# Performance work log

Measured on AMD Instinct MI355X. Metric: run time of the kernel, lower is better.

## Reference

```python
import jax, jax.numpy as jnp
import numpy as np

T, B, D, H, A = 256, 512, 128, 128, 8
RUN_COUNT = 1000

def _orth(k, shape, scale):
    w = jax.random.normal(k, shape, jnp.float32)
    q, r = jnp.linalg.qr(w)
    q = q * jnp.sign(jnp.diag(r))[None, :]
    return scale * q

def setup_inputs() -> dict:
    key = jax.random.key(0)
    ks = jax.random.split(key, 12)
    return {
        'hidden': jnp.zeros((B, H), jnp.float32),
        'obs': jax.random.normal(ks[0], (T, B, D), jnp.float32),
        'dones': (jax.random.randint(ks[1], (T, B), 0, 10) == 0),
        'mean_obs': jax.random.normal(ks[2], (D,), jnp.float32) * 0.1,
        'welford_S': jax.random.uniform(ks[3], (D,), jnp.float32) * RUN_COUNT,
        'running_count': RUN_COUNT,
        'W_emb': _orth(ks[4], (D, H), float(np.sqrt(2.0))), 'b_emb': jnp.zeros((H,), jnp.float32),
        'Wi': jax.random.normal(ks[5], (H, 3 * H), jnp.float32) / np.sqrt(H),
        'Wh': jax.random.normal(ks[6], (H, 3 * H), jnp.float32) / np.sqrt(H),
        'bh': jnp.zeros((3 * H,), jnp.float32),
        'W_act': _orth(ks[7], (H, H), 2.0), 'b_act': jnp.zeros((H,), jnp.float32),
        'W_alpha': _orth(ks[8], (H, A), 0.01), 'b_alpha': jnp.zeros((A,), jnp.float32),
        'W_beta': _orth(ks[9], (H, A), 0.01), 'b_beta': jnp.zeros((A,), jnp.float32),
    }

def _welford(M0, S0, count0, xs):
    # sequential Welford update over stacked rows, as in the original lax.scan
    def step(carry, x):
        M, S, c = carry
        c = c + 1.0
        M_new = M + (x - M) / c
        S_new = S + (x - M) * (x - M_new)
        return (M_new, S_new, c), None
    (M, S, c), _ = jax.lax.scan(step, (M0, S0, jnp.asarray(count0, jnp.float32)), xs)
    return M, S, c

def reference(hidden, obs, dones, mean_obs, welford_S, running_count,
              W_emb, b_emb, Wi, Wh, bh, W_act, b_act, W_alpha, b_alpha, W_beta, b_beta):
    # --- running-stat normalization (running_count > 0 branch) ---
    stacked = obs.reshape(-1, obs.shape[-1])  # [T*B, D]
    M, S, c = _welford(mean_obs, welford_S, running_count, stacked)
    var = S / (c - 1.0)
    obs_n = (obs - M) / (jnp.sqrt(var) + 1e-8)
    # --- embedding MLP ---
    emb = jax.nn.relu(obs_n @ W_emb + b_emb)  # [T, B, H]
    # --- GRU scan over time; precompute input-side gate projections (no input bias, flax GRUCell) ---
    xg = emb @ Wi  # [T, B, 3H]
    def gru_step(h, inp):
        x3, reset = inp
        h = jnp.where(reset[:, None], 0.0, h)  # reset carry where done
        hg = h @ Wh + bh
        xr, xz, xn = jnp.split(x3, 3, axis=-1)
        hr, hz, hn = jnp.split(hg, 3, axis=-1)
        r = jax.nn.sigmoid(xr + hr)
        z = jax.nn.sigmoid(xz + hz)
        n = jnp.tanh(xn + r * hn)
        h_new = (1.0 - z) * n + z * h
        return h_new, h_new
    h_last, ys = jax.lax.scan(gru_step, hidden, (xg, dones))  # ys: [T, B, H]
    # --- policy heads ---
    act = jax.nn.relu(ys @ W_act + b_act)
    alpha = jax.nn.softplus(act @ W_alpha + b_alpha) + 1.0
    beta = jax.nn.softplus(act @ W_beta + b_beta) + 1.0
    return h_last, alpha, beta, M, S
```

## Files before the change

### kernel.cpp

```cpp
#include <hip/hip_runtime.h>

#define T_DIM 256
#define B_DIM 512
#define D_DIM 128
#define H_DIM 128
#define A_DIM 8
#define N_ROWS (T_DIM*B_DIM)
#define NT (N_ROWS/16)
#define NWIN 8
#define WLEN 32
#define LOG2E 1.4426950408889634f

typedef __attribute__((ext_vector_type(4))) float f32x4;
typedef __attribute__((ext_vector_type(8))) short bf16x8;
typedef __attribute__((ext_vector_type(4))) short bf16x4;
typedef __attribute__((ext_vector_type(8))) _Float16 f16x8;
typedef __attribute__((ext_vector_type(4))) unsigned u32x4;
typedef __attribute__((ext_vector_type(2))) unsigned u32x2;

#define OFF_PSUM   0ull
#define OFF_PSQ    1048576ull
#define OFF_STATM  2097152ull
#define OFF_STATI  2097664ull
#define OFF_WEMB   2098176ull
#define OFF_WI     2130944ull
#define OFF_WH     2229248ull
#define OFF_WACT   2425856ull
#define OFF_WHEAD  2458624ull
#define OFF_TLO    2462720ull
#define OFF_UH     2464768ull
#define OFF_XG     4194304ull
#define OFF_YS     104857600ull

#define OUT_H      0
#define OUT_ALPHA  65536
#define OUT_BETA   1114112
#define OUT_M      2162688
#define OUT_S      2162816

__device__ inline short f2bf(float x){
  union { float f; unsigned u; } v; v.f = x;
  unsigned r = v.u + 0x7FFFu + ((v.u>>16)&1u);
  return (short)(r>>16);
}
__device__ inline float bf2f(short h){
  union { unsigned u; float f; } v; v.u = ((unsigned)(unsigned short)h)<<16; return v.f;
}

__device__ inline int swz(int row, int col){ return row*136 + col; }

__device__ inline unsigned cvtpk_bf16(float lo, float hi){
  unsigned r;
  asm("v_cvt_pk_bf16_f32 %0, %1, %2" : "=v"(r) : "v"(lo), "v"(hi));
  return r;
}

__global__ __launch_bounds__(256) void k_partial(const float* __restrict__ obs,
                                                 double* __restrict__ psum,
                                                 double* __restrict__ psq){
  int tid = threadIdx.x; int col = tid & 127; int rh = tid >> 7;
  double s = 0.0, q = 0.0;
  for (int r = blockIdx.x*2 + rh; r < N_ROWS; r += 2048){
    float v = obs[(size_t)r*D_DIM + col];
    s += (double)v; q += (double)v*(double)v;
  }
  __shared__ double ls[256], lq[256];
  ls[tid]=s; lq[tid]=q; __syncthreads();
  if (rh==0){
    psum[(size_t)blockIdx.x*128 + col] = ls[tid] + ls[tid+128];
    psq [(size_t)blockIdx.x*128 + col] = lq[tid] + lq[tid+128];
  }
}

__global__ __launch_bounds__(1024) void k_stats(const double* __restrict__ psum,
                                                const double* __restrict__ psq,
                                                const float* __restrict__ mean_obs,
                                                const float* __restrict__ welfS,
                                                const int* __restrict__ runcnt,
                                                float* __restrict__ outM, float* __restrict__ outS,
                                                float* __restrict__ wsM,  float* __restrict__ wsI){
  int tid = threadIdx.x; int col = tid & 127; int seg = tid >> 7;
  double s=0.0, q=0.0;
  for (int b=seg; b<1024; b+=8){ s += psum[(size_t)b*128+col]; q += psq[(size_t)b*128+col]; }
  __shared__ double ls[1024], lq[1024];
  ls[tid]=s; lq[tid]=q; __syncthreads();
  if (seg==0){
    for (int b=1;b<8;b++){ s += ls[b*128+col]; q += lq[b*128+col]; }
    double c0 = (double)runcnt[0];
    double Nn = (double)N_ROWS;
    double n  = c0 + Nn;
    double M0 = (double)mean_obs[col], S0 = (double)welfS[col];
    double mb = s / Nn;
    double delta = mb - M0;
    double M = M0 + delta * Nn / n;
    double M2b = q - Nn*mb*mb;
    double S = S0 + M2b + delta*delta*c0*Nn/n;
    double var = S / (n - 1.0);
    float inv = (float)(1.0/(sqrt(var)+1e-8));
    outM[col] = (float)M; outS[col] = (float)S;
    wsM[col]  = (float)M; wsI[col]  = inv;
  }
}

__global__ void k_pack_all(const float* __restrict__ W_emb, const float* __restrict__ Wi,
                           const float* __restrict__ Wh,    const float* __restrict__ W_act,
                           const float* __restrict__ W_al,  const float* __restrict__ W_be,
                           short* __restrict__ Bemb, short* __restrict__ BWi,
                           short* __restrict__ BWh,  short* __restrict__ Bact,
                           short* __restrict__ Bhead){
  int gidx = blockIdx.x*256 + threadIdx.x;
  if (gidx >= 133120) return;
  if (gidx >= 131072){
    int idx = gidx - 131072;
    int j = idx & 7, lane = (idx>>3)&63, kb = (idx>>9)&3;
    int k = kb*32 + (lane>>4)*8 + j;
    int n = lane & 15;
    float wv = (n<8) ? W_al[(size_t)k*8 + n] : W_be[(size_t)k*8 + (n-8)];
    Bhead[idx] = f2bf(wv);
    return;
  }
  const float* src; short* dst; int C; int fmt; int idx;
  if (gidx < 16384)      { src=W_emb; dst=Bemb; C=128; fmt=0; idx=gidx; }
  else if (gidx < 65536) { src=Wi;    dst=BWi;  C=384; fmt=0; idx=gidx-16384; }
  else if (gidx < 114688){ src=Wh;    dst=BWh;  C=384; fmt=1; idx=gidx-65536; }
  else                   { src=W_act; dst=Bact; C=128; fmt=0; idx=gidx-114688; }
  int j = idx & 7, lane = (idx>>3)&63, kb = (idx>>9)&3, ct = idx>>11;
  int k = kb*32 + (lane>>4)*8 + j;
  int n = ct*16 + (lane&15);
  float wv = src[(size_t)k*C + n];
  short h;
  if (fmt==0) h = f2bf(wv);
  else {
    wv *= (n < 256) ? LOG2E : (2.f*LOG2E);
    union { _Float16 hf; short s; } u; u.hf = (_Float16)wv; h = u.s;
  }
  dst[idx] = h;
}

__global__ __launch_bounds__(512) void k_sched(const unsigned char* __restrict__ dones,
                                               int* __restrict__ tlo,
                                               unsigned char* __restrict__ usehid){
  int k = blockIdx.x;
  int b = threadIdx.x;
  int t0 = 0, uh = 1;
  if (k > 0){
    for (int t = WLEN*k; t >= 0; t--){
      if (dones[(size_t)t*B_DIM + b]){ t0 = t; uh = 0; break; }
    }
  }
  usehid[k*B_DIM + b] = (unsigned char)uh;
  __shared__ int red[512];
  red[b] = t0; __syncthreads();
  if (b < 32){
    int m = red[b*16];
    #pragma unroll
    for (int i=1;i<16;i++) m = min(m, red[b*16+i]);
    tlo[k*32 + b] = m;
  }
}

__global__ __launch_bounds__(256) void k_embxg(const float* __restrict__ obs,
                                               const float* __restrict__ wsM,
                                               const float* __restrict__ wsI,
                                               const short* __restrict__ Bemb,
                                               const float* __restrict__ b_emb,
                                               const short* __restrict__ BWi,
                                               const float* __restrict__ bh,
                                               short* __restrict__ xgpk){
  int tid=threadIdx.x, w=tid>>6, lane=tid&63, q=lane>>4, l=lane&15;
  int rt = blockIdx.x*4 + w;
  int r0 = rt*16;
  __shared__ __align__(16) short L[4][16*136];
  short* Lw = &L[w][0];

  {
    int row = lane>>2, c0 = (lane&3)*32;
    const float* op = obs + (size_t)(r0+row)*D_DIM + c0;
    #pragma unroll
    for (int it=0; it<8; it++){
      f32x4 o = *(const f32x4*)(op + it*4);
      f32x4 m = *(const f32x4*)(wsM + c0 + it*4);
      f32x4 iv= *(const f32x4*)(wsI + c0 + it*4);
      bf16x4 v;
      v[0]=f2bf((o[0]-m[0])*iv[0]); v[1]=f2bf((o[1]-m[1])*iv[1]);
      v[2]=f2bf((o[2]-m[2])*iv[2]); v[3]=f2bf((o[3]-m[3])*iv[3]);
      *(bf16x4*)&Lw[swz(row, c0+it*4)] = v;
    }
  }
  asm volatile("s_waitcnt lgkmcnt(0)" ::: "memory");

  bf16x8 A[4];
  #pragma unroll
  for (int kb=0;kb<4;kb++) A[kb] = *(const bf16x8*)&Lw[swz(l, kb*32+q*8)];
  asm volatile("s_waitcnt lgkmcnt(0)" ::: "memory");

  const bf16x8* BE = (const bf16x8*)Bemb;
  #pragma unroll
  for (int ct=0; ct<8; ct++){
    f32x4 acc = {0.f,0.f,0.f,0.f};
    #pragma unroll
    for (int kb=0;kb<4;kb++)
      acc = __builtin_amdgcn_mfma_f32_16x16x32_bf16(A[kb], BE[(ct*4+kb)*64+lane], acc, 0,0,0);
    float bb = b_emb[ct*16 + l];
    #pragma unroll
    for (int r2=0;r2<4;r2++){
      float e = acc[r2] + bb; e = e>0.f ? e : 0.f;
      Lw[swz(q*4+r2, ct*16+l)] = f2bf(e);
    }
  }
  asm volatile("s_waitcnt lgkmcnt(0)" ::: "memory");

  bf16x8 A2[4];
  #pragma unroll
  for (int kb=0;kb<4;kb++) A2[kb] = *(const bf16x8*)&Lw[swz(l, kb*32+q*8)];
  asm volatile("s_waitcnt lgkmcnt(0)" ::: "memory");

  const bf16x8* BW = (const bf16x8*)BWi;
  u32x2* xg8 = (u32x2*)xgpk;
  #pragma unroll
  for (int g=0; g<3; g++){
    #pragma unroll
    for (int c8=0; c8<8; c8++){
      int ct = g*8 + c8;
      f32x4 acc = {0.f,0.f,0.f,0.f};
      #pragma unroll
      for (int kb=0;kb<4;kb++)
        acc = __builtin_amdgcn_mfma_f32_16x16x32_bf16(A2[kb], BW[(ct*4+kb)*64+lane], acc, 0,0,0);
      int col = ct*16 + l;
      float bb = (g<2) ? bh[col] : 0.f;
      float sc = (g<2) ? LOG2E : (2.f*LOG2E);
      u32x2 pv;
      pv[0] = cvtpk_bf16((acc[0]+bb)*sc, (acc[1]+bb)*sc);
      pv[1] = cvtpk_bf16((acc[2]+bb)*sc, (acc[3]+bb)*sc);
      xg8[((size_t)rt*24 + ct)*64 + lane] = pv;
    }
  }
}

#define LDB(g,kb) __builtin_bit_cast(f16x8, pw4[(((g)*8+w)*4+(kb))*64+lane])
__global__
__attribute__((amdgpu_flat_work_group_size(512,512)))
__attribute__((amdgpu_waves_per_eu(2,2)))
void k_gru(const float* __restrict__ hidden,
           const unsigned char* __restrict__ dones,
           const short* __restrict__ xgpk,
           const short* __restrict__ BWh,
           const float* __restrict__ bh,
           const int* __restrict__ tlo,
           const unsigned char* __restrict__ usehid,
           short* __restrict__ yspk,
           float* __restrict__ h_last){
  int tid=threadIdx.x, w=tid>>6, lane=tid&63, q=lane>>4, l=lane&15;
  int kk = blockIdx.x >> 5, bt = blockIdx.x & 31;
  int t_out0 = kk*WLEN;
  int t_end  = t_out0 + WLEN;
  int t_start = tlo[kk*32 + bt];

  __shared__ __align__(16) _Float16 hF[2][16*136];

  const u32x4* pw4 = (const u32x4*)BWh;
  f16x8 B00 = LDB(0,0), B01 = LDB(0,1), B02 = LDB(0,2), B03 = LDB(0,3);
  f16x8 B10 = LDB(1,0), B11 = LDB(1,1), B12 = LDB(1,2), B13 = LDB(1,3);
  f16x8 B20 = LDB(2,0), B21 = LDB(2,1), B22 = LDB(2,2), B23 = LDB(2,3);

  float bh2c = bh[2*128 + w*16 + l] * (2.f*LOG2E);

  float hv[4];
  #pragma unroll
  for (int r2=0;r2<4;r2++){
    int b = bt*16 + q*4 + r2;
    hv[r2] = usehid[kk*B_DIM + b] ? hidden[(size_t)b*H_DIM + w*16 + l] : 0.f;
  }

  const bf16x4* xgt = (const bf16x4*)xgpk + (((size_t)t_start*32 + bt)*24 + w)*64 + lane;
  const unsigned char* dnp = dones + (size_t)t_start*B_DIM + bt*16 + q*4;
  bf16x4* yst = (bf16x4*)yspk + (((size_t)t_start*32 + bt)*8 + w)*64 + lane;

  bf16x4 xr_c = xgt[0], xz_c = xgt[512], xn_c = xgt[1024];
  unsigned dn_c = *(const unsigned*)dnp;
  { int a1 = (t_start+1 < t_end) ? 1 : 0; xgt += (size_t)a1*49152; dnp += a1*B_DIM; }
  bf16x4 xr_n = xgt[0], xz_n = xgt[512], xn_n = xgt[1024];
  unsigned dn_n = *(const unsigned*)dnp;

  _Float16* hA = &hF[0][0];
  _Float16* hB = &hF[1][0];
  const int wo = q*4*136 + w*16 + l;
  const int ro = l*136 + q*8;

  for (int t = t_start; t < t_end; t++){
    #pragma unroll
    for (int r2=0;r2<4;r2++){
      float hvv = ((dn_c >> (r2*8)) & 255u) ? 0.f : hv[r2];
      hv[r2] = hvv;
      hA[wo + r2*136] = (_Float16)hvv;
    }
    asm volatile("s_waitcnt lgkmcnt(0)" ::: "memory");
    __builtin_amdgcn_s_barrier();
    asm volatile("" ::: "memory");

    int a2 = (t+2 < t_end) ? 1 : 0;
    xgt += (size_t)a2 * 49152;
    dnp += a2 * B_DIM;
    bf16x4 xr_2 = xgt[0], xz_2 = xgt[512], xn_2 = xgt[1024];
    unsigned dn_2 = *(const unsigned*)dnp;

    f16x8 A0 = *(const f16x8*)(hA + ro +  0);
    f16x8 A1 = *(const f16x8*)(hA + ro + 32);
    f16x8 A2 = *(const f16x8*)(hA + ro + 64);
    f16x8 A3 = *(const f16x8*)(hA + ro + 96);

    f32x4 acc0 = {0.f,0.f,0.f,0.f}, acc1 = {0.f,0.f,0.f,0.f}, acc2 = {0.f,0.f,0.f,0.f};
    acc0 = __builtin_amdgcn_mfma_f32_16x16x32_f16(A0, B00, acc0, 0,0,0);
    acc1 = __builtin_amdgcn_mfma_f32_16x16x32_f16(A0, B10, acc1, 0,0,0);
    acc2 = __builtin_amdgcn_mfma_f32_16x16x32_f16(A0, B20, acc2, 0,0,0);
    acc0 = __builtin_amdgcn_mfma_f32_16x16x32_f16(A1, B01, acc0, 0,0,0);
    acc1 = __builtin_amdgcn_mfma_f32_16x16x32_f16(A1, B11, acc1, 0,0,0);
    acc2 = __builtin_amdgcn_mfma_f32_16x16x32_f16(A1, B21, acc2, 0,0,0);
    acc0 = __builtin_amdgcn_mfma_f32_16x16x32_f16(A2, B02, acc0, 0,0,0);
    acc1 = __builtin_amdgcn_mfma_f32_16x16x32_f16(A2, B12, acc1, 0,0,0);
    acc2 = __builtin_amdgcn_mfma_f32_16x16x32_f16(A2, B22, acc2, 0,0,0);
    acc0 = __builtin_amdgcn_mfma_f32_16x16x32_f16(A3, B03, acc0, 0,0,0);
    acc1 = __builtin_amdgcn_mfma_f32_16x16x32_f16(A3, B13, acc1, 0,0,0);
    acc2 = __builtin_amdgcn_mfma_f32_16x16x32_f16(A3, B23, acc2, 0,0,0);

    #pragma unroll
    for (int r2=0;r2<4;r2++){
      float xr = bf2f(xr_c[r2]), xz = bf2f(xz_c[r2]), xn = bf2f(xn_c[r2]);
      float rg = __builtin_amdgcn_rcpf(1.f + __builtin_amdgcn_exp2f(-(xr + acc0[r2])));
      float zg = __builtin_amdgcn_rcpf(1.f + __builtin_amdgcn_exp2f(-(xz + acc1[r2])));
      float e2 = __builtin_amdgcn_exp2f(xn + rg*(acc2[r2] + bh2c));
      float ng = 1.f - 2.f*__builtin_amdgcn_rcpf(e2 + 1.f);
      hv[r2] = ng + zg*(hv[r2] - ng);
    }
    if (t >= t_out0){
      u32x2 pv;
      pv[0] = cvtpk_bf16(hv[0], hv[1]);
      pv[1] = cvtpk_bf16(hv[2], hv[3]);
      *(u32x2*)yst = pv;
    }
    yst += 16384;
    xr_c = xr_n; xz_c = xz_n; xn_c = xn_n; dn_c = dn_n;
    xr_n = xr_2; xz_n = xz_2; xn_n = xn_2; dn_n = dn_2;
    _Float16* tmp = hA; hA = hB; hB = tmp;
  }

  if (kk == NWIN-1){
    #pragma unroll
    for (int r2=0;r2<4;r2++)
      h_last[(size_t)(bt*16+q*4+r2)*H_DIM + w*16 + l] = hv[r2];
  }
}

__global__ __launch_bounds__(256) void k_heads(const short* __restrict__ yspk,
                                               const short* __restrict__ Bact,
                                               const float* __restrict__ b_act,
                                               const short* __restrict__ Bhead,
                                               const float* __restrict__ b_alpha,
                                               const float* __restrict__ b_beta,
                                               float* __restrict__ alpha,
                                               float* __restrict__ beta){
  int tid=threadIdx.x, w=tid>>6, lane=tid&63, q=lane>>4, l=lane&15;
  size_t rt = (size_t)blockIdx.x*4 + w;
  __shared__ __align__(16) short tl[4][16*136];
  short* Lw = &tl[w][0];
  const bf16x4* ys4 = (const bf16x4*)yspk;
  #pragma unroll
  for (int ct=0; ct<8; ct++){
    bf16x4 v = ys4[(rt*8+ct)*64+lane];
    #pragma unroll
    for (int r2=0;r2<4;r2++) Lw[swz(q*4+r2, ct*16+l)] = v[r2];
  }
  asm volatile("s_waitcnt lgkmcnt(0)" ::: "memory");
  bf16x8 A[4];
  #pragma unroll
  for (int kb=0;kb<4;kb++) A[kb] = *(const bf16x8*)&Lw[swz(l, kb*32+q*8)];
  asm volatile("s_waitcnt lgkmcnt(0)" ::: "memory");
  const bf16x8* BA = (const bf16x8*)Bact;
  #pragma unroll
  for (int ct=0;ct<8;ct++){
    f32x4 acc = {0.f,0.f,0.f,0.f};
    #pragma unroll
    for (int kb=0;kb<4;kb++)
      acc = __builtin_amdgcn_mfma_f32_16x16x32_bf16(A[kb], BA[(ct*4+kb)*64+lane], acc, 0,0,0);
    int col = ct*16 + l;
    float bb = b_act[col];
    #pragma unroll
    for (int r2=0;r2<4;r2++){
      float e = acc[r2] + bb; e = e>0.f ? e : 0.f;
      Lw[swz(q*4+r2, col)] = f2bf(e);
    }
  }
  asm volatile("s_waitcnt lgkmcnt(0)" ::: "memory");
  bf16x8 A2[4];
  #pragma unroll
  for (int kb=0;kb<4;kb++) A2[kb] = *(const bf16x8*)&Lw[swz(l, kb*32+q*8)];
  asm volatile("s_waitcnt lgkmcnt(0)" ::: "memory");
  const bf16x8* BHd = (const bf16x8*)Bhead;
  f32x4 acc = {0.f,0.f,0.f,0.f};
  #pragma unroll
  for (int kb=0;kb<4;kb++)
    acc = __builtin_amdgcn_mfma_f32_16x16x32_bf16(A2[kb], BHd[kb*64+lane], acc, 0,0,0);
  float bb = (l<8) ? b_alpha[l] : b_beta[l-8];
  float* dst = (l<8) ? alpha : beta;
  int cc = (l<8) ? l : l-8;
  #pragma unroll
  for (int r2=0;r2<4;r2++){
    float u = acc[r2] + bb;
    float e = __builtin_amdgcn_exp2f(-fabsf(u)*LOG2E);
    float sp = fmaxf(u,0.f) + 0.6931471805599453f*__builtin_amdgcn_logf(1.f + e);
    dst[(rt*16 + q*4 + r2)*8 + cc] = sp + 1.f;
  }
}

extern "C" void kernel_launch(void* const* d_in, const int* in_sizes, int n_in,
                              void* d_out, int out_size, void* d_ws, size_t ws_size,
                              hipStream_t stream){
  const float* hidden   = (const float*)d_in[0];
  const float* obs      = (const float*)d_in[1];
  const unsigned char* dones = (const unsigned char*)d_in[2];
  const float* mean_obs = (const float*)d_in[3];
  const float* welfS    = (const float*)d_in[4];
  const int*   runcnt   = (const int*)d_in[5];
  const float* W_emb = (const float*)d_in[6];
  const float* b_emb = (const float*)d_in[7];
  const float* Wi    = (const float*)d_in[8];
  const float* Wh    = (const float*)d_in[9];
  const float* bh    = (const float*)d_in[10];
  const float* W_act = (const float*)d_in[11];
  const float* b_act = (const float*)d_in[12];
  const float* W_al  = (const float*)d_in[13];
  const float* b_al  = (const float*)d_in[14];
  const float* W_be  = (const float*)d_in[15];
  const float* b_be  = (const float*)d_in[16];
  float* out = (float*)d_out;
  char*  ws  = (char*)d_ws;

  double* psum = (double*)(ws + OFF_PSUM);
  double* psq  = (double*)(ws + OFF_PSQ);
  float*  wsM  = (float*)(ws + OFF_STATM);
  float*  wsI  = (float*)(ws + OFF_STATI);
  short*  Bemb = (short*)(ws + OFF_WEMB);
  short*  BWi  = (short*)(ws + OFF_WI);
  short*  BWh  = (short*)(ws + OFF_WH);
  short*  Bact = (short*)(ws + OFF_WACT);
  short*  Bhead= (short*)(ws + OFF_WHEAD);
  int*    tlo  = (int*)(ws + OFF_TLO);
  unsigned char* uh = (unsigned char*)(ws + OFF_UH);
  short*  xgpk = (short*)(ws + OFF_XG);
  short*  yspk = (short*)(ws + OFF_YS);

  k_partial<<<1024,256,0,stream>>>(obs, psum, psq);
  k_stats<<<1,1024,0,stream>>>(psum, psq, mean_obs, welfS, runcnt,
                               out+OUT_M, out+OUT_S, wsM, wsI);
  k_sched<<<NWIN,512,0,stream>>>(dones, tlo, uh);
  k_pack_all<<<520,256,0,stream>>>(W_emb, Wi, Wh, W_act, W_al, W_be,
                                   Bemb, BWi, BWh, Bact, Bhead);
  k_embxg<<<2048,256,0,stream>>>(obs, wsM, wsI, Bemb, b_emb, BWi, bh, xgpk);
  k_gru<<<NWIN*32,512,0,stream>>>(hidden, dones, xgpk, BWh, bh, tlo, uh,
                                  yspk, out + OUT_H);
  k_heads<<<2048,256,0,stream>>>(yspk, Bact, b_act, Bhead, b_al, b_be,
                                 out + OUT_ALPHA, out + OUT_BETA);
}
```

Measured before the change: 511.3 us.

## Stage weights in LDS and process four row tiles per wave in embxg and heads

The embedding/input-projection kernel and the heads kernel now copy their packed weight matrices into shared memory once per block. Each wave then handles four 16-row tiles, so one block covers 16 tiles instead of 4. This cuts repeated global/L2 weight fetches per tile and the grid drops to a quarter of its former size. In exchange it uses more LDS per block (lower occupancy), adds block barriers and keeps more register state (a2 holds four tiles of activations), which can raise register pressure.

New measurement: 502.1 us. Within noise of the previous version (-1.8%).

```diff
diff --git a/kernel.cpp b/kernel.cpp
--- a/kernel.cpp
+++ b/kernel.cpp
@@ -168,72 +168,97 @@
                                                const float* __restrict__ bh,
                                                short* __restrict__ xgpk){
   int tid=threadIdx.x, w=tid>>6, lane=tid&63, q=lane>>4, l=lane&15;
-  int rt = blockIdx.x*4 + w;
-  int r0 = rt*16;
-  __shared__ __align__(16) short L[4][16*136];
-  short* Lw = &L[w][0];
+  __shared__ __align__(16) short Wlds[16384];
+  __shared__ __align__(16) short scratch[4][16*136];
+
+  short* Lw = &scratch[w][0];
+  int rt0 = blockIdx.x*16 + w*4;
 
   {
-    int row = lane>>2, c0 = (lane&3)*32;
-    const float* op = obs + (size_t)(r0+row)*D_DIM + c0;
-    #pragma unroll
-    for (int it=0; it<8; it++){
-      f32x4 o = *(const f32x4*)(op + it*4);
-      f32x4 m = *(const f32x4*)(wsM + c0 + it*4);
-      f32x4 iv= *(const f32x4*)(wsI + c0 + it*4);
-      bf16x4 v;
-      v[0]=f2bf((o[0]-m[0])*iv[0]); v[1]=f2bf((o[1]-m[1])*iv[1]);
-      v[2]=f2bf((o[2]-m[2])*iv[2]); v[3]=f2bf((o[3]-m[3])*iv[3]);
-      *(bf16x4*)&Lw[swz(row, c0+it*4)] = v;
-    }
-  }
-  asm volatile("s_waitcnt lgkmcnt(0)" ::: "memory");
-
-  bf16x8 A[4];
+    u32x4* dst = (u32x4*)Wlds;
+    const u32x4* src = (const u32x4*)Bemb;
+    #pragma unroll
+    for (int i=0;i<8;i++) dst[tid + i*256] = src[tid + i*256];
+  }
+  __syncthreads();
+
+  bf16x8 a2[4][4];
   #pragma unroll
-  for (int kb=0;kb<4;kb++) A[kb] = *(const bf16x8*)&Lw[swz(l, kb*32+q*8)];
-  asm volatile("s_waitcnt lgkmcnt(0)" ::: "memory");
-
-  const bf16x8* BE = (const bf16x8*)Bemb;
-  #pragma unroll
-  for (int ct=0; ct<8; ct++){
-    f32x4 acc = {0.f,0.f,0.f,0.f};
-    #pragma unroll
-    for (int kb=0;kb<4;kb++)
-      acc = __builtin_amdgcn_mfma_f32_16x16x32_bf16(A[kb], BE[(ct*4+kb)*64+lane], acc, 0,0,0);
-    float bb = b_emb[ct*16 + l];
-    #pragma unroll
-    for (int r2=0;r2<4;r2++){
-      float e = acc[r2] + bb; e = e>0.f ? e : 0.f;
-      Lw[swz(q*4+r2, ct*16+l)] = f2bf(e);
-    }
-  }
-  asm volatile("s_waitcnt lgkmcnt(0)" ::: "memory");
-
-  bf16x8 A2[4];
-  #pragma unroll
-  for (int kb=0;kb<4;kb++) A2[kb] = *(const bf16x8*)&Lw[swz(l, kb*32+q*8)];
-  asm volatile("s_waitcnt lgkmcnt(0)" ::: "memory");
-
-  const bf16x8* BW = (const bf16x8*)BWi;
+  for (int tt=0; tt<4; tt++){
+    int rt = rt0 + tt;
+    int r0 = rt*16;
+    {
+      int row = lane>>2, c0 = (lane&3)*32;
+      const float* op = obs + (size_t)(r0+row)*D_DIM + c0;
+      #pragma unroll
+      for (int it=0; it<8; it++){
+        f32x4 o = *(const f32x4*)(op + it*4);
+        f32x4 m = *(const f32x4*)(wsM + c0 + it*4);
+        f32x4 iv= *(const f32x4*)(wsI + c0 + it*4);
+        bf16x4 v;
+        v[0]=f2bf((o[0]-m[0])*iv[0]); v[1]=f2bf((o[1]-m[1])*iv[1]);
+        v[2]=f2bf((o[2]-m[2])*iv[2]); v[3]=f2bf((o[3]-m[3])*iv[3]);
+        *(bf16x4*)&Lw[swz(row, c0+it*4)] = v;
+      }
+    }
+    asm volatile("s_waitcnt lgkmcnt(0)" ::: "memory");
+    bf16x8 A[4];
+    #pragma unroll
+    for (int kb=0;kb<4;kb++) A[kb] = *(const bf16x8*)&Lw[swz(l, kb*32+q*8)];
+    asm volatile("s_waitcnt lgkmcnt(0)" ::: "memory");
+    #pragma unroll
+    for (int ct=0; ct<8; ct++){
+      f32x4 acc = {0.f,0.f,0.f,0.f};
+      #pragma unroll
+      for (int kb=0;kb<4;kb++)
+        acc = __builtin_amdgcn_mfma_f32_16x16x32_bf16(A[kb],
+                *(const bf16x8*)&Wlds[((ct*4+kb)*64+lane)*8], acc, 0,0,0);
+      float bb = b_emb[ct*16 + l];
+      #pragma unroll
+      for (int r2=0;r2<4;r2++){
+        float e = acc[r2] + bb; e = e>0.f ? e : 0.f;
+        Lw[swz(q*4+r2, ct*16+l)] = f2bf(e);
+      }
+    }
+    asm volatile("s_waitcnt lgkmcnt(0)" ::: "memory");
+    #pragma unroll
+    for (int kb=0;kb<4;kb++) a2[tt][kb] = *(const bf16x8*)&Lw[swz(l, kb*32+q*8)];
+    asm volatile("s_waitcnt lgkmcnt(0)" ::: "memory");
+  }
+  __syncthreads();
+
   u32x2* xg8 = (u32x2*)xgpk;
-  #pragma unroll
   for (int g=0; g<3; g++){
-    #pragma unroll
-    for (int c8=0; c8<8; c8++){
-      int ct = g*8 + c8;
-      f32x4 acc = {0.f,0.f,0.f,0.f};
-      #pragma unroll
-      for (int kb=0;kb<4;kb++)
-        acc = __builtin_amdgcn_mfma_f32_16x16x32_bf16(A2[kb], BW[(ct*4+kb)*64+lane], acc, 0,0,0);
-      int col = ct*16 + l;
-      float bb = (g<2) ? bh[col] : 0.f;
-      float sc = (g<2) ? LOG2E : (2.f*LOG2E);
-      u32x2 pv;
-      pv[0] = cvtpk_bf16((acc[0]+bb)*sc, (acc[1]+bb)*sc);
-      pv[1] = cvtpk_bf16((acc[2]+bb)*sc, (acc[3]+bb)*sc);
-      xg8[((size_t)rt*24 + ct)*64 + lane] = pv;
-    }
+    {
+      u32x4* dst = (u32x4*)Wlds;
+      const u32x4* src = (const u32x4*)BWi + (size_t)g*2048;
+      #pragma unroll
+      for (int i=0;i<8;i++) dst[tid + i*256] = src[tid + i*256];
+    }
+    __syncthreads();
+    float sc = (g<2) ? LOG2E : (2.f*LOG2E);
+    float bb = (g<2) ? bh[g*128 ] : 0.f;
+    #pragma unroll
+    for (int tt=0; tt<4; tt++){
+      int rt = rt0 + tt;
+      #pragma unroll
+      for (int j=0; j<8; j++){
+        int ct = g*8 + j;
+        f32x4 acc = {0.f,0.f,0.f,0.f};
+        #pragma unroll
+        for (int kb=0;kb<4;kb++)
+          acc = __builtin_amdgcn_mfma_f32_16x16x32_bf16(a2[tt][kb],
+                  *(const bf16x8*)&Wlds[((j*4+kb)*64+lane)*8], acc, 0,0,0);
+        int col = ct*16 + l;
+        float bv = (g<2) ? bh[col] : 0.f;
+        u32x2 pv;
+        pv[0] = cvtpk_bf16((acc[0]+bv)*sc, (acc[1]+bv)*sc);
+        pv[1] = cvtpk_bf16((acc[2]+bv)*sc, (acc[3]+bv)*sc);
+        xg8[((size_t)rt*24 + ct)*64 + lane] = pv;
+      }
+    }
+    if (g < 2) __syncthreads();
+    (void)bb;
   }
 }
 
@@ -360,55 +385,71 @@
                                                float* __restrict__ alpha,
                                                float* __restrict__ beta){
   int tid=threadIdx.x, w=tid>>6, lane=tid&63, q=lane>>4, l=lane&15;
-  size_t rt = (size_t)blockIdx.x*4 + w;
-  __shared__ __align__(16) short tl[4][16*136];
-  short* Lw = &tl[w][0];
+  __shared__ __align__(16) short Wlds[16384];
+  __shared__ __align__(16) short Hlds[2048];
+  __shared__ __align__(16) short scratch[4][16*136];
+  short* Lw = &scratch[w][0];
+  size_t rt0 = (size_t)blockIdx.x*16 + w*4;
+
+  {
+    u32x4* dst = (u32x4*)Wlds;
+    const u32x4* src = (const u32x4*)Bact;
+    #pragma unroll
+    for (int i=0;i<8;i++) dst[tid + i*256] = src[tid + i*256];
+    ((u32x4*)Hlds)[tid] = ((const u32x4*)Bhead)[tid];
+  }
+  __syncthreads();
+
   const bf16x4* ys4 = (const bf16x4*)yspk;
   #pragma unroll
-  for (int ct=0; ct<8; ct++){
-    bf16x4 v = ys4[(rt*8+ct)*64+lane];
-    #pragma unroll
-    for (int r2=0;r2<4;r2++) Lw[swz(q*4+r2, ct*16+l)] = v[r2];
-  }
-  asm volatile("s_waitcnt lgkmcnt(0)" ::: "memory");
-  bf16x8 A[4];
-  #pragma unroll
-  for (int kb=0;kb<4;kb++) A[kb] = *(const bf16x8*)&Lw[swz(l, kb*32+q*8)];
-  asm volatile("s_waitcnt lgkmcnt(0)" ::: "memory");
-  const bf16x8* BA = (const bf16x8*)Bact;
-  #pragma unroll
-  for (int ct=0;ct<8;ct++){
+  for (int tt=0; tt<4; tt++){
+    size_t rt = rt0 + tt;
+    #pragma unroll
+    for (int ct=0; ct<8; ct++){
+      bf16x4 v = ys4[(rt*8+ct)*64+lane];
+      #pragma unroll
+      for (int r2=0;r2<4;r2++) Lw[swz(q*4+r2, ct*16+l)] = v[r2];
+    }
+    asm volatile("s_waitcnt lgkmcnt(0)" ::: "memory");
+    bf16x8 A[4];
+    #pragma unroll
+    for (int kb=0;kb<4;kb++) A[kb] = *(const bf16x8*)&Lw[swz(l, kb*32+q*8)];
+    asm volatile("s_waitcnt lgkmcnt(0)" ::: "memory");
+    #pragma unroll
+    for (int ct=0;ct<8;ct++){
+      f32x4 acc = {0.f,0.f,0.f,0.f};
+      #pragma unroll
+      for (int kb=0;kb<4;kb++)
+        acc = __builtin_amdgcn_mfma_f32_16x16x32_bf16(A[kb],
+                *(const bf16x8*)&Wlds[((ct*4+kb)*64+lane)*8], acc, 0,0,0);
+      int col = ct*16 + l;
+      float bb = b_act[col];
+      #pragma unroll
+      for (int r2=0;r2<4;r2++){
+        float e = acc[r2] + bb; e = e>0.f ? e : 0.f;
+        Lw[swz(q*4+r2, col)] = f2bf(e);
+      }
+    }
+    asm volatile("s_waitcnt lgkmcnt(0)" ::: "memory");
+    bf16x8 A2[4];
+    #pragma unroll
+    for (int kb=0;kb<4;kb++) A2[kb] = *(const bf16x8*)&Lw[swz(l, kb*32+q*8)];
+    asm volatile("s_waitcnt lgkmcnt(0)" ::: "memory");
     f32x4 acc = {0.f,0.f,0.f,0.f};
     #pragma unroll
     for (int kb=0;kb<4;kb++)
-      acc = __builtin_amdgcn_mfma_f32_16x16x32_bf16(A[kb], BA[(ct*4+kb)*64+lane], acc, 0,0,0);
-    int col = ct*16 + l;
-    float bb = b_act[col];
+      acc = __builtin_amdgcn_mfma_f32_16x16x32_bf16(A2[kb],
+              *(const bf16x8*)&Hlds[(kb*64+lane)*8], acc, 0,0,0);
+    float bb = (l<8) ? b_alpha[l] : b_beta[l-8];
+    float* dst = (l<8) ? alpha : beta;
+    int cc = (l<8) ? l : l-8;
     #pragma unroll
     for (int r2=0;r2<4;r2++){
-      float e = acc[r2] + bb; e = e>0.f ? e : 0.f;
-      Lw[swz(q*4+r2, col)] = f2bf(e);
-    }
-  }
-  asm volatile("s_waitcnt lgkmcnt(0)" ::: "memory");
-  bf16x8 A2[4];
-  #pragma unroll
-  for (int kb=0;kb<4;kb++) A2[kb] = *(const bf16x8*)&Lw[swz(l, kb*32+q*8)];
-  asm volatile("s_waitcnt lgkmcnt(0)" ::: "memory");
-  const bf16x8* BHd = (const bf16x8*)Bhead;
-  f32x4 acc = {0.f,0.f,0.f,0.f};
-  #pragma unroll
-  for (int kb=0;kb<4;kb++)
-    acc = __builtin_amdgcn_mfma_f32_16x16x32_bf16(A2[kb], BHd[kb*64+lane], acc, 0,0,0);
-  float bb = (l<8) ? b_alpha[l] : b_beta[l-8];
-  float* dst = (l<8) ? alpha : beta;
-  int cc = (l<8) ? l : l-8;
-  #pragma unroll
-  for (int r2=0;r2<4;r2++){
-    float u = acc[r2] + bb;
-    float e = __builtin_amdgcn_exp2f(-fabsf(u)*LOG2E);
-    float sp = fmaxf(u,0.f) + 0.6931471805599453f*__builtin_amdgcn_logf(1.f + e);
-    dst[(rt*16 + q*4 + r2)*8 + cc] = sp + 1.f;
+      float u = acc[r2] + bb;
+      float e = __builtin_amdgcn_exp2f(-fabsf(u)*LOG2E);
+      float sp = fmaxf(u,0.f) + 0.6931471805599453f*__builtin_amdgcn_logf(1.f + e);
+      dst[(rt*16 + q*4 + r2)*8 + cc] = sp + 1.f;
+    }
   }
 }
 
@@ -455,9 +496,9 @@
   k_sched<<<NWIN,512,0,stream>>>(dones, tlo, uh);
   k_pack_all<<<520,256,0,stream>>>(W_emb, Wi, Wh, W_act, W_al, W_be,
                                    Bemb, BWi, BWh, Bact, Bhead);
-  k_embxg<<<2048,256,0,stream>>>(obs, wsM, wsI, Bemb, b_emb, BWi, bh, xgpk);
+  k_embxg<<<512,256,0,stream>>>(obs, wsM, wsI, Bemb, b_emb, BWi, bh, xgpk);
   k_gru<<<NWIN*32,512,0,stream>>>(hidden, dones, xgpk, BWh, bh, tlo, uh,
                                   yspk, out + OUT_H);
-  k_heads<<<2048,256,0,stream>>>(yspk, Bact, b_act, Bhead, b_al, b_be,
-                                 out + OUT_ALPHA, out + OUT_BETA);
-}
+  k_heads<<<512,256,0,stream>>>(yspk, Bact, b_act, Bhead, b_al, b_be,
+                                out + OUT_ALPHA, out + OUT_BETA);
+}
```
